# Kernel optimization log

Measured on AMD Instinct MI355X. Metric: run time of the kernel, lower is better.

Reference implementation:

```python
import jax, jax.numpy as jnp
import numpy as np

B, STATE_DIM, ACTION_DIM = 16384, 512, 64
HID, NQ, QED = 1024, 64, 64
EPS = 1e-5


def _layernorm(x, gamma, beta):
    mu = jnp.mean(x, axis=-1, keepdims=True)
    var = jnp.mean(jnp.square(x - mu), axis=-1, keepdims=True)
    return (x - mu) * jax.lax.rsqrt(var + EPS) * gamma + beta


def setup_inputs() -> dict:
    key = jax.random.key(0)
    ks = jax.random.split(key, 12)
    s = 0.02  # small init scale for stable activations
    return {
        "state": jax.random.normal(ks[0], (B, STATE_DIM), jnp.float32),
        "action": jax.random.normal(ks[1], (B, ACTION_DIM), jnp.float32),
        "W1": jax.random.normal(ks[2], (STATE_DIM + ACTION_DIM, HID), jnp.float32) * s,
        "b1": jax.random.normal(ks[3], (HID,), jnp.float32) * s,
        "g1": jnp.ones((HID,), jnp.float32),
        "be1": jnp.zeros((HID,), jnp.float32),
        "W2": jax.random.normal(ks[4], (HID, HID), jnp.float32) * s,
        "b2": jax.random.normal(ks[5], (HID,), jnp.float32) * s,
        "g2": jnp.ones((HID,), jnp.float32),
        "be2": jnp.zeros((HID,), jnp.float32),
        "Wq1": jax.random.normal(ks[6], (1, QED), jnp.float32) * s,
        "bq1": jax.random.normal(ks[7], (QED,), jnp.float32) * s,
        "Wq2": jax.random.normal(ks[8], (QED, QED), jnp.float32) * s,
        "bq2": jax.random.normal(ks[9], (QED,), jnp.float32) * s,
        "Wh": jax.random.normal(ks[10], (HID + QED, 1), jnp.float32) * s,
        "bh": jax.random.normal(ks[11], (1,), jnp.float32) * s,
    }


def reference(state, action, W1, b1, g1, be1, W2, b2, g2, be2,
              Wq1, bq1, Wq2, bq2, Wh, bh):
    # tau buffer: midpoints of NQ uniform bins
    tau = jnp.linspace(0.0, 1.0, NQ + 1)[:-1] + 1.0 / (2 * NQ)  # [NQ]

    # feature_net (Dropout is identity in eval)
    x = jnp.concatenate([state, action], axis=-1)               # [B, S+A]
    h = jax.nn.relu(_layernorm(x @ W1 + b1, g1, be1))           # [B, HID]
    h = jax.nn.relu(_layernorm(h @ W2 + b2, g2, be2))           # [B, HID]

    # quantile embedding: tau rows are batch-independent -> one [NQ, QED] MLP
    te = jax.nn.relu(tau[:, None] @ Wq1 + bq1) @ Wq2 + bq2      # [NQ, QED]

    # head on concat([features, tau_emb]) == split the head weight
    Wf, Wt = Wh[:HID, 0], Wh[HID:, 0]                           # [HID], [QED]
    quantiles = h @ Wf[:, None] + (te @ Wt)[None, :] + bh[0]    # [B, NQ]
    return quantiles
```

## Files before the change

### kernel.cpp

```cpp
#include <hip/hip_runtime.h>
#include <hip/hip_bf16.h>
#include <cstddef>

#define B_ROWS 16384
#define SDIM 512
#define ADIM 64
#define KDIM 576
#define HID 1024
#define NQ 64

#define T1_BLOCKS ((KDIM / 32) * (HID / 32))
#define T2_BLOCKS ((HID / 32) * (HID / 32))
#define PREP_BLOCKS (T1_BLOCKS + T2_BLOCKS + 1)

#define FK_LDS (16384 + 131072)

typedef __attribute__((ext_vector_type(8))) __bf16 bf16x8;
typedef __attribute__((ext_vector_type(4))) float f32x4;

static __device__ __forceinline__ float bf2f(unsigned short u) {
  union { unsigned int i; float f; } x; x.i = ((unsigned int)u) << 16; return x.f;
}
static __device__ __forceinline__ unsigned short f2bf(float f) {
  union { float f; unsigned int i; } x; x.f = f;
  unsigned int i = x.i + (0x7fffu + ((x.i >> 16) & 1u));
  return (unsigned short)(i >> 16);
}

static __device__ __forceinline__ void gload_lds16(const unsigned short* g, unsigned short* l) {
  __builtin_amdgcn_global_load_lds(
      (const __attribute__((address_space(1))) void*)(const void*)g,
      (__attribute__((address_space(3))) void*)(void*)l, 16, 0, 0);
}

static __device__ __forceinline__ uint4 pack8(float4 a, float4 b) {
  uint4 o;
  o.x = (unsigned)f2bf(a.x) | ((unsigned)f2bf(a.y) << 16);
  o.y = (unsigned)f2bf(a.z) | ((unsigned)f2bf(a.w) << 16);
  o.z = (unsigned)f2bf(b.x) | ((unsigned)f2bf(b.y) << 16);
  o.w = (unsigned)f2bf(b.z) | ((unsigned)f2bf(b.w) << 16);
  return o;
}

static __device__ __forceinline__ void transpose_body(
    const float* __restrict__ W, unsigned short* __restrict__ Wb,
    int Kin, int N, int k0, int n0, unsigned short* tile) {
  const int tx = threadIdx.x & 31, ty = threadIdx.x >> 5;
#pragma unroll
  for (int i = 0; i < 32; i += 8)
    tile[(ty + i) * 33 + tx] = f2bf(W[(size_t)(k0 + ty + i) * N + n0 + tx]);
  __syncthreads();
#pragma unroll
  for (int i = 0; i < 32; i += 8)
    Wb[(size_t)(n0 + ty + i) * Kin + k0 + tx] = tile[tx * 33 + ty + i];
}

__global__ __launch_bounds__(256) void prep_k(
    const float* __restrict__ W1, const float* __restrict__ W2,
    const float* __restrict__ Wq1, const float* __restrict__ bq1,
    const float* __restrict__ Wq2, const float* __restrict__ bq2,
    const float* __restrict__ Wh, const float* __restrict__ bh,
    unsigned short* __restrict__ w1b, unsigned short* __restrict__ w2b,
    float* __restrict__ qoff) {
  __shared__ unsigned short tile[32 * 33];
  const int b = blockIdx.x;
  if (b < T1_BLOCKS) {
    transpose_body(W1, w1b, KDIM, HID, (b / 32) * 32, (b % 32) * 32, tile);
  } else if (b < T1_BLOCKS + T2_BLOCKS) {
    const int t = b - T1_BLOCKS;
    transpose_body(W2, w2b, HID, HID, (t / 32) * 32, (t % 32) * 32, tile);
  } else {
    const int q = threadIdx.x;
    if (q < NQ) {
      const float tau = ((float)q + 0.5f) * (1.0f / (float)NQ);
      float t1[64];
#pragma unroll
      for (int k = 0; k < 64; ++k) t1[k] = fmaxf(fmaf(tau, Wq1[k], bq1[k]), 0.f);
      float acc = bh[0];
#pragma unroll 1
      for (int j = 0; j < 64; ++j) {
        float t2 = bq2[j];
#pragma unroll
        for (int k = 0; k < 64; ++k) t2 = fmaf(t1[k], Wq2[k * 64 + j], t2);
        acc = fmaf(t2, Wh[HID + j], acc);
      }
      qoff[q] = acc;
    }
  }
}

template <bool XSRC, bool FINAL>
__global__ __launch_bounds__(512, 2) void fused_k(
    const float* __restrict__ Xs,
    const float* __restrict__ Xa,
    const unsigned short* __restrict__ A,
    const unsigned short* __restrict__ Bt,
    const float* __restrict__ bias, const float* __restrict__ g,
    const float* __restrict__ be, const float* __restrict__ Wh,
    const float* __restrict__ qoff,
    unsigned short* __restrict__ Hout, float* __restrict__ Qout,
    int K, int NT) {
  extern __shared__ unsigned short sm[];
  __shared__ float part[8][64][2];
  __shared__ float murs[64][2];
  __shared__ float dotf[64];
  __shared__ float qof[64];

  const int tid = threadIdx.x;
  const int w = tid >> 6, l = tid & 63;
  const int r0 = (int)blockIdx.x * 64;
  const int sb = (int)blockIdx.x % NT;

  const int sce = ((((l & 7) << 4) ^ (((l >> 3) & 4) << 3)) >> 1);
  const int lr = (l & 15) << 7;
  const int cSw = (((l >> 4) << 4) ^ ((l & 4) << 3));

  f32x4 acc[4][8] = {};
  float4 ar0, ar1;

#define KT(x) ((((x) + sb) % NT) << 6)
#define AF(d, mi, kk) (*(const bf16x8*)(sm + (((d)*8192 + (mi)*2048 + lr + cSw + ((kk) << 6)) >> 1)))
#define BFW(ni, kk) (*(const bf16x8*)(sm + ((16384 + w*16384 + (ni)*2048 + lr + cSw + ((kk) << 6)) >> 1)))
#define ISSUE_A(d, kt) \
    gload_lds16(A + (size_t)(r0 + w * 8 + (l >> 3)) * K + (kt) + sce, \
                sm + (((d)*8192 + w * 1024) >> 1))
#define ALOADX(kt) do { \
    const int row_ = r0 + w * 8 + (l >> 3); \
    if ((kt) < SDIM) { const float* p_ = Xs + (size_t)row_ * SDIM + (kt) + sce; \
      ar0 = *(const float4*)p_; ar1 = *(const float4*)(p_ + 4); } \
    else { const float* p_ = Xa + (size_t)row_ * ADIM + ((kt) - SDIM) + sce; \
      ar0 = *(const float4*)p_; ar1 = *(const float4*)(p_ + 4); } } while (0)
#define AWRX(d) (*(uint4*)(sm + (((d)*8192 + w * 1024 + l * 16) >> 1)) = pack8(ar0, ar1))
#define ISSUE_B(kt) do { _Pragma("unroll") for (int i_ = 0; i_ < 16; ++i_) \
    gload_lds16(Bt + (size_t)(w * 128 + i_ * 8 + (l >> 3)) * K + (kt) + sce, \
                sm + ((16384 + w * 16384 + i_ * 1024) >> 1)); } while (0)
#define BAR() __builtin_amdgcn_s_barrier()
#define WAITLGKM() asm volatile("s_waitcnt lgkmcnt(0)" ::: "memory")
#define WAITVM(n) asm volatile("s_waitcnt vmcnt(" #n ")" ::: "memory")

  if (XSRC) {
    ALOADX(KT(0)); AWRX(0);
    ISSUE_B(KT(0));
    if (NT > 1) ALOADX(KT(1));
    WAITLGKM(); BAR();
  } else {
    ISSUE_A(0, KT(0));
    ISSUE_B(KT(0));
    ISSUE_A(1, KT(1));
    WAITVM(17); BAR();
  }

  for (int t = 0; t < NT; ++t) {
    const int d = t & 1;
    if (t + 1 < NT) { if (XSRC) { WAITVM(2); } else { WAITVM(1); } }
    else { WAITVM(0); }
    bf16x8 af[4], bfr[8];
#pragma unroll
    for (int mi = 0; mi < 4; ++mi) af[mi] = AF(d, mi, 0);
#pragma unroll
    for (int ni = 0; ni < 8; ++ni) bfr[ni] = BFW(ni, 0);
    __builtin_amdgcn_s_setprio(1);
#pragma unroll
    for (int mi = 0; mi < 4; ++mi)
#pragma unroll
      for (int ni = 0; ni < 8; ++ni)
        acc[mi][ni] = __builtin_amdgcn_mfma_f32_16x16x32_bf16(af[mi], bfr[ni], acc[mi][ni], 0, 0, 0);
    __builtin_amdgcn_s_setprio(0);
#pragma unroll
    for (int mi = 0; mi < 4; ++mi) af[mi] = AF(d, mi, 1);
#pragma unroll
    for (int ni = 0; ni < 8; ++ni) bfr[ni] = BFW(ni, 1);
    WAITLGKM();
    if (t + 1 < NT) ISSUE_B(KT(t + 1));
    if (XSRC && t + 1 < NT) AWRX((t + 1) & 1);
    __builtin_amdgcn_s_setprio(1);
#pragma unroll
    for (int mi = 0; mi < 4; ++mi)
#pragma unroll
      for (int ni = 0; ni < 8; ++ni)
        acc[mi][ni] = __builtin_amdgcn_mfma_f32_16x16x32_bf16(af[mi], bfr[ni], acc[mi][ni], 0, 0, 0);
    __builtin_amdgcn_s_setprio(0);
    if (XSRC) {
      if (t + 1 < NT) { WAITLGKM(); }
      BAR();
      if (t + 2 < NT) ALOADX(KT(t + 2));
    } else {
      if (t + 1 < NT) { WAITVM(16); }
      BAR();
      if (t + 2 < NT) ISSUE_A(d, KT(t + 2));
    }
  }

  float bcol[8], gcol[8], becol[8];
#pragma unroll
  for (int ni = 0; ni < 8; ++ni) {
    const int col = w * 128 + ni * 16 + (l & 15);
    bcol[ni] = bias[col];
    gcol[ni] = g[col];
    becol[ni] = be[col];
  }
#pragma unroll
  for (int mi = 0; mi < 4; ++mi)
#pragma unroll
    for (int rr = 0; rr < 4; ++rr) {
      float s1 = 0.f, s2 = 0.f;
#pragma unroll
      for (int ni = 0; ni < 8; ++ni) {
        const float x = acc[mi][ni][rr] + bcol[ni];
        s1 += x; s2 += x * x;
      }
#pragma unroll
      for (int o = 1; o < 16; o <<= 1) {
        s1 += __shfl_xor(s1, o, 64);
        s2 += __shfl_xor(s2, o, 64);
      }
      if ((l & 15) == 0) {
        const int row = mi * 16 + (l >> 4) * 4 + rr;
        part[w][row][0] = s1;
        part[w][row][1] = s2;
      }
    }
  __syncthreads();
  if (tid < 64) {
    float s1 = 0.f, s2 = 0.f;
#pragma unroll
    for (int ww = 0; ww < 8; ++ww) { s1 += part[ww][tid][0]; s2 += part[ww][tid][1]; }
    const float mu = s1 * (1.0f / HID);
    murs[tid][0] = mu;
    murs[tid][1] = rsqrtf(s2 * (1.0f / HID) - mu * mu + 1e-5f);
    if (FINAL) qof[tid] = qoff[tid];
  }
  __syncthreads();

  if (!FINAL) {
#pragma unroll
    for (int mi = 0; mi < 4; ++mi)
#pragma unroll
      for (int rr = 0; rr < 4; ++rr) {
        const int row = mi * 16 + (l >> 4) * 4 + rr;
        const float mu = murs[row][0], rs = murs[row][1];
        unsigned short* hp = Hout + (size_t)(r0 + row) * HID + w * 128 + (l & 15);
#pragma unroll
        for (int ni = 0; ni < 8; ++ni) {
          const float x = acc[mi][ni][rr] + bcol[ni];
          hp[ni * 16] = f2bf(fmaxf((x - mu) * rs * gcol[ni] + becol[ni], 0.f));
        }
      }
  } else {
    float wf[8];
#pragma unroll
    for (int ni = 0; ni < 8; ++ni) wf[ni] = Wh[w * 128 + ni * 16 + (l & 15)];
#pragma unroll
    for (int mi = 0; mi < 4; ++mi)
#pragma unroll
      for (int rr = 0; rr < 4; ++rr) {
        const int row = mi * 16 + (l >> 4) * 4 + rr;
        const float mu = murs[row][0], rs = murs[row][1];
        float dp = 0.f;
#pragma unroll
        for (int ni = 0; ni < 8; ++ni) {
          const float x = acc[mi][ni][rr] + bcol[ni];
          dp += fmaxf((x - mu) * rs * gcol[ni] + becol[ni], 0.f) * wf[ni];
        }
#pragma unroll
        for (int o = 1; o < 16; o <<= 1) dp += __shfl_xor(dp, o, 64);
        if ((l & 15) == 0) part[w][row][0] = dp;
      }
    __syncthreads();
    if (tid < 64) {
      float dsum = 0.f;
#pragma unroll
      for (int ww = 0; ww < 8; ++ww) dsum += part[ww][tid][0];
      dotf[tid] = dsum;
    }
    __syncthreads();
#pragma unroll
    for (int it = 0; it < 8; ++it) {
      const int idx = tid + it * 512;
      const int row = idx >> 6, q = idx & 63;
      Qout[(size_t)(r0 + row) * NQ + q] = dotf[row] + qof[q];
    }
  }
#undef KT
#undef AF
#undef BFW
#undef ISSUE_A
#undef ALOADX
#undef AWRX
#undef ISSUE_B
#undef BAR
#undef WAITLGKM
#undef WAITVM
}

extern "C" void kernel_launch(void* const* d_in, const int* in_sizes, int n_in,
                              void* d_out, int out_size, void* d_ws, size_t ws_size,
                              hipStream_t stream) {
  const float* state  = (const float*)d_in[0];
  const float* action = (const float*)d_in[1];
  const float* W1  = (const float*)d_in[2];
  const float* b1  = (const float*)d_in[3];
  const float* g1  = (const float*)d_in[4];
  const float* be1 = (const float*)d_in[5];
  const float* W2  = (const float*)d_in[6];
  const float* b2  = (const float*)d_in[7];
  const float* g2  = (const float*)d_in[8];
  const float* be2 = (const float*)d_in[9];
  const float* Wq1 = (const float*)d_in[10];
  const float* bq1 = (const float*)d_in[11];
  const float* Wq2 = (const float*)d_in[12];
  const float* bq2 = (const float*)d_in[13];
  const float* Wh  = (const float*)d_in[14];
  const float* bh  = (const float*)d_in[15];
  float* out = (float*)d_out;

  char* ws = (char*)d_ws;
  size_t off = 0;
  float* qoff = (float*)(ws + off); off += 256;
  unsigned short* w1b = (unsigned short*)(ws + off); off += (size_t)HID * KDIM * 2;
  unsigned short* w2b = (unsigned short*)(ws + off); off += (size_t)HID * HID * 2;
  unsigned short* h1b = (unsigned short*)(ws + off);

  (void)hipFuncSetAttribute((const void*)fused_k<true, false>, hipFuncAttributeMaxDynamicSharedMemorySize, FK_LDS);
  (void)hipFuncSetAttribute((const void*)fused_k<false, true>, hipFuncAttributeMaxDynamicSharedMemorySize, FK_LDS);

  prep_k<<<PREP_BLOCKS, 256, 0, stream>>>(W1, W2, Wq1, bq1, Wq2, bq2, Wh, bh,
                                          w1b, w2b, qoff);

  fused_k<true, false><<<B_ROWS / 64, 512, FK_LDS, stream>>>(
      state, action, nullptr, w1b, b1, g1, be1, nullptr, nullptr,
      h1b, nullptr, KDIM, KDIM / 64);
  fused_k<false, true><<<B_ROWS / 64, 512, FK_LDS, stream>>>(
      nullptr, nullptr, h1b, w2b, b2, g2, be2, Wh, qoff,
      nullptr, out, HID, HID / 64);
}
```

Before: 107.8 us.

## Load B fragments directly into registers and deepen A pipeline to eight stages

B-operand fragments are now read straight from global memory into registers, double-buffered by k-half, instead of being staged through LDS. This cuts LDS from about 144 KB to 64 KB. The freed LDS holds an 8-slot A ring with 4 tiles of lookahead and a barrier only every fourth K-step. NT becomes a template parameter so the loop can be fully unrolled. The cost is uncoalesced per-lane B loads from L2 and higher register pressure, since launch_bounds no longer asks for 2 blocks per SM.

```diff
diff --git a/kernel.cpp b/kernel.cpp
--- a/kernel.cpp
+++ b/kernel.cpp
@@ -13,7 +13,7 @@
 #define T2_BLOCKS ((HID / 32) * (HID / 32))
 #define PREP_BLOCKS (T1_BLOCKS + T2_BLOCKS + 1)
 
-#define FK_LDS (16384 + 131072)
+#define FK_LDS 65536
 
 typedef __attribute__((ext_vector_type(8))) __bf16 bf16x8;
 typedef __attribute__((ext_vector_type(4))) float f32x4;
@@ -89,8 +89,8 @@
   }
 }
 
-template <bool XSRC, bool FINAL>
-__global__ __launch_bounds__(512, 2) void fused_k(
+template <bool XSRC, bool FINAL, int NT>
+__global__ __launch_bounds__(512) void fused_k(
     const float* __restrict__ Xs,
     const float* __restrict__ Xa,
     const unsigned short* __restrict__ A,
@@ -99,7 +99,7 @@
     const float* __restrict__ be, const float* __restrict__ Wh,
     const float* __restrict__ qoff,
     unsigned short* __restrict__ Hout, float* __restrict__ Qout,
-    int K, int NT) {
+    int K) {
   extern __shared__ unsigned short sm[];
   __shared__ float part[8][64][2];
   __shared__ float murs[64][2];
@@ -116,81 +116,83 @@
   const int cSw = (((l >> 4) << 4) ^ ((l & 4) << 3));
 
   f32x4 acc[4][8] = {};
-  float4 ar0, ar1;
+  bf16x8 b0[8], b1[8];
+  float4 ar0, ar1, br0, br1;
+
+  const unsigned short* Bp = Bt + (size_t)(w * 128 + (l & 15)) * K + ((l >> 4) << 3);
 
 #define KT(x) ((((x) + sb) % NT) << 6)
 #define AF(d, mi, kk) (*(const bf16x8*)(sm + (((d)*8192 + (mi)*2048 + lr + cSw + ((kk) << 6)) >> 1)))
-#define BFW(ni, kk) (*(const bf16x8*)(sm + ((16384 + w*16384 + (ni)*2048 + lr + cSw + ((kk) << 6)) >> 1)))
 #define ISSUE_A(d, kt) \
     gload_lds16(A + (size_t)(r0 + w * 8 + (l >> 3)) * K + (kt) + sce, \
                 sm + (((d)*8192 + w * 1024) >> 1))
-#define ALOADX(kt) do { \
+#define ALOADX(q0, q1, kt) do { \
     const int row_ = r0 + w * 8 + (l >> 3); \
     if ((kt) < SDIM) { const float* p_ = Xs + (size_t)row_ * SDIM + (kt) + sce; \
-      ar0 = *(const float4*)p_; ar1 = *(const float4*)(p_ + 4); } \
+      q0 = *(const float4*)p_; q1 = *(const float4*)(p_ + 4); } \
     else { const float* p_ = Xa + (size_t)row_ * ADIM + ((kt) - SDIM) + sce; \
-      ar0 = *(const float4*)p_; ar1 = *(const float4*)(p_ + 4); } } while (0)
-#define AWRX(d) (*(uint4*)(sm + (((d)*8192 + w * 1024 + l * 16) >> 1)) = pack8(ar0, ar1))
-#define ISSUE_B(kt) do { _Pragma("unroll") for (int i_ = 0; i_ < 16; ++i_) \
-    gload_lds16(Bt + (size_t)(w * 128 + i_ * 8 + (l >> 3)) * K + (kt) + sce, \
-                sm + ((16384 + w * 16384 + i_ * 1024) >> 1)); } while (0)
+      q0 = *(const float4*)p_; q1 = *(const float4*)(p_ + 4); } } while (0)
+#define AWRX(d, q0, q1) (*(uint4*)(sm + (((d)*8192 + w * 1024 + l * 16) >> 1)) = pack8(q0, q1))
+#define LOADB(dst, kt, kk) do { _Pragma("unroll") for (int ni = 0; ni < 8; ++ni) \
+    dst[ni] = *(const bf16x8*)(Bp + (size_t)(ni * 16) * K + (kt) + (kk) * 32); } while (0)
 #define BAR() __builtin_amdgcn_s_barrier()
 #define WAITLGKM() asm volatile("s_waitcnt lgkmcnt(0)" ::: "memory")
-#define WAITVM(n) asm volatile("s_waitcnt vmcnt(" #n ")" ::: "memory")
+#define WAITVM16() asm volatile("s_waitcnt vmcnt(16)" ::: "memory")
 
   if (XSRC) {
-    ALOADX(KT(0)); AWRX(0);
-    ISSUE_B(KT(0));
-    if (NT > 1) ALOADX(KT(1));
+    ALOADX(ar0, ar1, KT(0)); ALOADX(br0, br1, KT(1));
+    AWRX(0, ar0, ar1);
+    ALOADX(ar0, ar1, KT(2));
+    AWRX(1, br0, br1);
+    ALOADX(br0, br1, KT(3));
+    AWRX(2, ar0, ar1);
+    AWRX(3, br0, br1);
+    LOADB(b0, KT(0), 0); LOADB(b1, KT(0), 1);
     WAITLGKM(); BAR();
   } else {
-    ISSUE_A(0, KT(0));
-    ISSUE_B(KT(0));
-    ISSUE_A(1, KT(1));
-    WAITVM(17); BAR();
-  }
-
+    ISSUE_A(0, KT(0)); ISSUE_A(1, KT(1)); ISSUE_A(2, KT(2)); ISSUE_A(3, KT(3));
+    LOADB(b0, KT(0), 0); LOADB(b1, KT(0), 1);
+    WAITVM16(); BAR();
+  }
+
+#pragma unroll
   for (int t = 0; t < NT; ++t) {
-    const int d = t & 1;
-    if (t + 1 < NT) { if (XSRC) { WAITVM(2); } else { WAITVM(1); } }
-    else { WAITVM(0); }
-    bf16x8 af[4], bfr[8];
+    const int d = t & 7;
+    bf16x8 af[4];
+    if (XSRC) {
+      if (t + 4 < NT) ALOADX(ar0, ar1, KT(t + 4));
+    } else {
+      if (t + 4 < NT) ISSUE_A((t + 4) & 7, KT(t + 4));
+    }
 #pragma unroll
     for (int mi = 0; mi < 4; ++mi) af[mi] = AF(d, mi, 0);
-#pragma unroll
-    for (int ni = 0; ni < 8; ++ni) bfr[ni] = BFW(ni, 0);
     __builtin_amdgcn_s_setprio(1);
 #pragma unroll
     for (int mi = 0; mi < 4; ++mi)
 #pragma unroll
       for (int ni = 0; ni < 8; ++ni)
-        acc[mi][ni] = __builtin_amdgcn_mfma_f32_16x16x32_bf16(af[mi], bfr[ni], acc[mi][ni], 0, 0, 0);
+        acc[mi][ni] = __builtin_amdgcn_mfma_f32_16x16x32_bf16(af[mi], b0[ni], acc[mi][ni], 0, 0, 0);
     __builtin_amdgcn_s_setprio(0);
+    if (t + 1 < NT) LOADB(b0, KT(t + 1), 0);
 #pragma unroll
     for (int mi = 0; mi < 4; ++mi) af[mi] = AF(d, mi, 1);
-#pragma unroll
-    for (int ni = 0; ni < 8; ++ni) bfr[ni] = BFW(ni, 1);
-    WAITLGKM();
-    if (t + 1 < NT) ISSUE_B(KT(t + 1));
-    if (XSRC && t + 1 < NT) AWRX((t + 1) & 1);
     __builtin_amdgcn_s_setprio(1);
 #pragma unroll
     for (int mi = 0; mi < 4; ++mi)
 #pragma unroll
       for (int ni = 0; ni < 8; ++ni)
-        acc[mi][ni] = __builtin_amdgcn_mfma_f32_16x16x32_bf16(af[mi], bfr[ni], acc[mi][ni], 0, 0, 0);
+        acc[mi][ni] = __builtin_amdgcn_mfma_f32_16x16x32_bf16(af[mi], b1[ni], acc[mi][ni], 0, 0, 0);
     __builtin_amdgcn_s_setprio(0);
-    if (XSRC) {
-      if (t + 1 < NT) { WAITLGKM(); }
+    if (t + 1 < NT) LOADB(b1, KT(t + 1), 1);
+    if (XSRC && t + 4 < NT) AWRX((t + 4) & 7, ar0, ar1);
+    if (((t & 3) == 3) && (t + 1 < NT)) {
+      if (XSRC) { WAITLGKM(); } 
+      WAITVM16();
       BAR();
-      if (t + 2 < NT) ALOADX(KT(t + 2));
-    } else {
-      if (t + 1 < NT) { WAITVM(16); }
-      BAR();
-      if (t + 2 < NT) ISSUE_A(d, KT(t + 2));
-    }
-  }
-
+    }
+  }
+
+  __syncthreads();
   float bcol[8], gcol[8], becol[8];
 #pragma unroll
   for (int ni = 0; ni < 8; ++ni) {
@@ -283,14 +285,13 @@
   }
 #undef KT
 #undef AF
-#undef BFW
 #undef ISSUE_A
 #undef ALOADX
 #undef AWRX
-#undef ISSUE_B
+#undef LOADB
 #undef BAR
 #undef WAITLGKM
-#undef WAITVM
+#undef WAITVM16
 }
 
 extern "C" void kernel_launch(void* const* d_in, const int* in_sizes, int n_in,
@@ -321,16 +322,18 @@
   unsigned short* w2b = (unsigned short*)(ws + off); off += (size_t)HID * HID * 2;
   unsigned short* h1b = (unsigned short*)(ws + off);
 
-  (void)hipFuncSetAttribute((const void*)fused_k<true, false>, hipFuncAttributeMaxDynamicSharedMemorySize, FK_LDS);
-  (void)hipFuncSetAttribute((const void*)fused_k<false, true>, hipFuncAttributeMaxDynamicSharedMemorySize, FK_LDS);
+  (void)hipFuncSetAttribute((const void*)fused_k<true, false, KDIM / 64>,
+                            hipFuncAttributeMaxDynamicSharedMemorySize, FK_LDS);
+  (void)hipFuncSetAttribute((const void*)fused_k<false, true, HID / 64>,
+                            hipFuncAttributeMaxDynamicSharedMemorySize, FK_LDS);
 
   prep_k<<<PREP_BLOCKS, 256, 0, stream>>>(W1, W2, Wq1, bq1, Wq2, bq2, Wh, bh,
                                           w1b, w2b, qoff);
 
-  fused_k<true, false><<<B_ROWS / 64, 512, FK_LDS, stream>>>(
+  fused_k<true, false, KDIM / 64><<<B_ROWS / 64, 512, FK_LDS, stream>>>(
       state, action, nullptr, w1b, b1, g1, be1, nullptr, nullptr,
-      h1b, nullptr, KDIM, KDIM / 64);
-  fused_k<false, true><<<B_ROWS / 64, 512, FK_LDS, stream>>>(
+      h1b, nullptr, KDIM);
+  fused_k<false, true, HID / 64><<<B_ROWS / 64, 512, FK_LDS, stream>>>(
       nullptr, nullptr, h1b, w2b, b2, g2, be2, Wh, qoff,
-      nullptr, out, HID, HID / 64);
-}
+      nullptr, out, HID);
+}
```

New measurement: 150.2 us. 1.39x slower.

## Fuse both MLP layers into one kernel, keeping hidden activations in LDS

Applied to the files above, without the earlier changes.

Merges the two GEMM+LayerNorm kernels into one. The first layer's normalized bf16 output for each 64-row tile stays in shared memory instead of going through global memory. The second GEMM streams W2 directly from global into registers, using a new permute kernel that lays W2 out in MFMA fragment order. This removes the h1 write and read round trip and one launch. The cost is an extra permute launch and second-layer B loads that are no longer staged in LDS, which may stall the MFMA pipeline on global latency.

```diff
diff --git a/kernel.cpp b/kernel.cpp
--- a/kernel.cpp
+++ b/kernel.cpp
@@ -8,6 +8,8 @@
 #define KDIM 576
 #define HID 1024
 #define NQ 64
+#define NT1 9
+#define NT2 16
 
 #define T1_BLOCKS ((KDIM / 32) * (HID / 32))
 #define T2_BLOCKS ((HID / 32) * (HID / 32))
@@ -89,17 +91,26 @@
   }
 }
 
-template <bool XSRC, bool FINAL>
-__global__ __launch_bounds__(512, 2) void fused_k(
-    const float* __restrict__ Xs,
-    const float* __restrict__ Xa,
-    const unsigned short* __restrict__ A,
-    const unsigned short* __restrict__ Bt,
-    const float* __restrict__ bias, const float* __restrict__ g,
-    const float* __restrict__ be, const float* __restrict__ Wh,
-    const float* __restrict__ qoff,
-    unsigned short* __restrict__ Hout, float* __restrict__ Qout,
-    int K, int NT) {
+__global__ __launch_bounds__(256) void w2perm_k(
+    const unsigned short* __restrict__ w2b, unsigned short* __restrict__ w2c) {
+  const int gt = blockIdx.x * 256 + threadIdx.x;
+  const int c = gt >> 6, l = gt & 63;
+  const int ni = c & 7, kk = (c >> 3) & 1, t = (c >> 4) & 15, w = c >> 8;
+  const int row = w * 128 + ni * 16 + (l & 15);
+  const int kcol = t * 64 + kk * 32 + ((l >> 4) << 3);
+  *(uint4*)(w2c + (size_t)gt * 8) = *(const uint4*)(w2b + (size_t)row * HID + kcol);
+}
+
+__global__ __launch_bounds__(512, 2) void fused_all_k(
+    const float* __restrict__ Xs, const float* __restrict__ Xa,
+    const unsigned short* __restrict__ B1t,
+    const unsigned short* __restrict__ w2c,
+    const float* __restrict__ b1, const float* __restrict__ g1,
+    const float* __restrict__ be1,
+    const float* __restrict__ b2, const float* __restrict__ g2,
+    const float* __restrict__ be2,
+    const float* __restrict__ Wh, const float* __restrict__ qoff,
+    float* __restrict__ Qout) {
   extern __shared__ unsigned short sm[];
   __shared__ float part[8][64][2];
   __shared__ float murs[64][2];
@@ -109,7 +120,7 @@
   const int tid = threadIdx.x;
   const int w = tid >> 6, l = tid & 63;
   const int r0 = (int)blockIdx.x * 64;
-  const int sb = (int)blockIdx.x % NT;
+  const int sb = (int)blockIdx.x % NT1;
 
   const int sce = ((((l & 7) << 4) ^ (((l >> 3) & 4) << 3)) >> 1);
   const int lr = (l & 15) << 7;
@@ -118,12 +129,9 @@
   f32x4 acc[4][8] = {};
   float4 ar0, ar1;
 
-#define KT(x) ((((x) + sb) % NT) << 6)
-#define AF(d, mi, kk) (*(const bf16x8*)(sm + (((d)*8192 + (mi)*2048 + lr + cSw + ((kk) << 6)) >> 1)))
-#define BFW(ni, kk) (*(const bf16x8*)(sm + ((16384 + w*16384 + (ni)*2048 + lr + cSw + ((kk) << 6)) >> 1)))
-#define ISSUE_A(d, kt) \
-    gload_lds16(A + (size_t)(r0 + w * 8 + (l >> 3)) * K + (kt) + sce, \
-                sm + (((d)*8192 + w * 1024) >> 1))
+#define KT(x) ((((x) + sb) % NT1) << 6)
+#define AF1(d, mi, kk) (*(const bf16x8*)(sm + (((d)*8192 + (mi)*2048 + lr + cSw + ((kk) << 6)) >> 1)))
+#define BF1(ni, kk) (*(const bf16x8*)(sm + ((16384 + w*16384 + ((l & 15) * 8 + (ni)) * 128 + (((l >> 4) << 4) ^ (((ni) & 4) << 3)) + ((kk) << 6)) >> 1)))
 #define ALOADX(kt) do { \
     const int row_ = r0 + w * 8 + (l >> 3); \
     if ((kt) < SDIM) { const float* p_ = Xs + (size_t)row_ * SDIM + (kt) + sce; \
@@ -131,74 +139,59 @@
     else { const float* p_ = Xa + (size_t)row_ * ADIM + ((kt) - SDIM) + sce; \
       ar0 = *(const float4*)p_; ar1 = *(const float4*)(p_ + 4); } } while (0)
 #define AWRX(d) (*(uint4*)(sm + (((d)*8192 + w * 1024 + l * 16) >> 1)) = pack8(ar0, ar1))
-#define ISSUE_B(kt) do { _Pragma("unroll") for (int i_ = 0; i_ < 16; ++i_) \
-    gload_lds16(Bt + (size_t)(w * 128 + i_ * 8 + (l >> 3)) * K + (kt) + sce, \
+#define ISSUE_B1(kt) do { _Pragma("unroll") for (int i_ = 0; i_ < 16; ++i_) \
+    gload_lds16(B1t + (size_t)(w * 128 + i_ * 8 + (l >> 3)) * KDIM + (kt) + sce, \
                 sm + ((16384 + w * 16384 + i_ * 1024) >> 1)); } while (0)
+#define AF2(t, mi, kk) (*(const bf16x8*)(sm + ((16384 + ((t) >> 1) * 16384 + ((t) & 1) * 8192 + (mi)*2048 + lr + cSw + ((kk) << 6)) >> 1)))
+#define LOADB2H(dst, t, kk, h) do { _Pragma("unroll") for (int j_ = 0; j_ < 4; ++j_) \
+    dst[j_] = *(const bf16x8*)(w2c + ((size_t)((((w * NT2 + (t)) * 2 + (kk)) * 8 + (h) * 4 + j_) * 64 + l) * 8)); } while (0)
+#define MQ1(bsrc) do { _Pragma("unroll") for (int mi = 0; mi < 4; ++mi) \
+    _Pragma("unroll") for (int ni = 0; ni < 8; ++ni) \
+      acc[mi][ni] = __builtin_amdgcn_mfma_f32_16x16x32_bf16(af[mi], bsrc[ni], acc[mi][ni], 0, 0, 0); } while (0)
+#define MQ2(cv, NO) do { _Pragma("unroll") for (int mi = 0; mi < 4; ++mi) \
+    _Pragma("unroll") for (int j_ = 0; j_ < 4; ++j_) \
+      acc[mi][(NO) + j_] = __builtin_amdgcn_mfma_f32_16x16x32_bf16(af2[mi], cv[j_], acc[mi][(NO) + j_], 0, 0, 0); } while (0)
 #define BAR() __builtin_amdgcn_s_barrier()
 #define WAITLGKM() asm volatile("s_waitcnt lgkmcnt(0)" ::: "memory")
 #define WAITVM(n) asm volatile("s_waitcnt vmcnt(" #n ")" ::: "memory")
-
-  if (XSRC) {
-    ALOADX(KT(0)); AWRX(0);
-    ISSUE_B(KT(0));
-    if (NT > 1) ALOADX(KT(1));
-    WAITLGKM(); BAR();
-  } else {
-    ISSUE_A(0, KT(0));
-    ISSUE_B(KT(0));
-    ISSUE_A(1, KT(1));
-    WAITVM(17); BAR();
-  }
-
-  for (int t = 0; t < NT; ++t) {
+#define PRIO1() __builtin_amdgcn_s_setprio(1)
+#define PRIO0() __builtin_amdgcn_s_setprio(0)
+
+  ALOADX(KT(0)); AWRX(0);
+  ISSUE_B1(KT(0));
+  ALOADX(KT(1));
+  WAITLGKM(); BAR();
+
+  for (int t = 0; t < NT1; ++t) {
     const int d = t & 1;
-    if (t + 1 < NT) { if (XSRC) { WAITVM(2); } else { WAITVM(1); } }
-    else { WAITVM(0); }
+    if (t + 1 < NT1) { WAITVM(2); } else { WAITVM(0); }
     bf16x8 af[4], bfr[8];
 #pragma unroll
-    for (int mi = 0; mi < 4; ++mi) af[mi] = AF(d, mi, 0);
-#pragma unroll
-    for (int ni = 0; ni < 8; ++ni) bfr[ni] = BFW(ni, 0);
-    __builtin_amdgcn_s_setprio(1);
-#pragma unroll
-    for (int mi = 0; mi < 4; ++mi)
-#pragma unroll
-      for (int ni = 0; ni < 8; ++ni)
-        acc[mi][ni] = __builtin_amdgcn_mfma_f32_16x16x32_bf16(af[mi], bfr[ni], acc[mi][ni], 0, 0, 0);
-    __builtin_amdgcn_s_setprio(0);
-#pragma unroll
-    for (int mi = 0; mi < 4; ++mi) af[mi] = AF(d, mi, 1);
-#pragma unroll
-    for (int ni = 0; ni < 8; ++ni) bfr[ni] = BFW(ni, 1);
+    for (int mi = 0; mi < 4; ++mi) af[mi] = AF1(d, mi, 0);
+#pragma unroll
+    for (int ni = 0; ni < 8; ++ni) bfr[ni] = BF1(ni, 0);
+    PRIO1(); MQ1(bfr); PRIO0();
+#pragma unroll
+    for (int mi = 0; mi < 4; ++mi) af[mi] = AF1(d, mi, 1);
+#pragma unroll
+    for (int ni = 0; ni < 8; ++ni) bfr[ni] = BF1(ni, 1);
     WAITLGKM();
-    if (t + 1 < NT) ISSUE_B(KT(t + 1));
-    if (XSRC && t + 1 < NT) AWRX((t + 1) & 1);
-    __builtin_amdgcn_s_setprio(1);
-#pragma unroll
-    for (int mi = 0; mi < 4; ++mi)
-#pragma unroll
-      for (int ni = 0; ni < 8; ++ni)
-        acc[mi][ni] = __builtin_amdgcn_mfma_f32_16x16x32_bf16(af[mi], bfr[ni], acc[mi][ni], 0, 0, 0);
-    __builtin_amdgcn_s_setprio(0);
-    if (XSRC) {
-      if (t + 1 < NT) { WAITLGKM(); }
-      BAR();
-      if (t + 2 < NT) ALOADX(KT(t + 2));
-    } else {
-      if (t + 1 < NT) { WAITVM(16); }
-      BAR();
-      if (t + 2 < NT) ISSUE_A(d, KT(t + 2));
-    }
+    if (t + 1 < NT1) ISSUE_B1(KT(t + 1));
+    if (t + 1 < NT1) AWRX((t + 1) & 1);
+    PRIO1(); MQ1(bfr); PRIO0();
+    if (t + 1 < NT1) { WAITLGKM(); }
+    BAR();
+    if (t + 2 < NT1) ALOADX(KT(t + 2));
   }
 
   float bcol[8], gcol[8], becol[8];
-#pragma unroll
-  for (int ni = 0; ni < 8; ++ni) {
-    const int col = w * 128 + ni * 16 + (l & 15);
-    bcol[ni] = bias[col];
-    gcol[ni] = g[col];
-    becol[ni] = be[col];
-  }
+  const int cb = w * 128 + (l & 15) * 8;
+  *(float4*)&bcol[0]  = *(const float4*)(b1 + cb);
+  *(float4*)&bcol[4]  = *(const float4*)(b1 + cb + 4);
+  *(float4*)&gcol[0]  = *(const float4*)(g1 + cb);
+  *(float4*)&gcol[4]  = *(const float4*)(g1 + cb + 4);
+  *(float4*)&becol[0] = *(const float4*)(be1 + cb);
+  *(float4*)&becol[4] = *(const float4*)(be1 + cb + 4);
 #pragma unroll
   for (int mi = 0; mi < 4; ++mi)
 #pragma unroll
@@ -228,66 +221,132 @@
     const float mu = s1 * (1.0f / HID);
     murs[tid][0] = mu;
     murs[tid][1] = rsqrtf(s2 * (1.0f / HID) - mu * mu + 1e-5f);
-    if (FINAL) qof[tid] = qoff[tid];
-  }
-  __syncthreads();
-
-  if (!FINAL) {
-#pragma unroll
-    for (int mi = 0; mi < 4; ++mi)
-#pragma unroll
-      for (int rr = 0; rr < 4; ++rr) {
+    qof[tid] = qoff[tid];
+  }
+  __syncthreads();
+#pragma unroll
+  for (int mi = 0; mi < 4; ++mi)
+#pragma unroll
+    for (int rr = 0; rr < 4; ++rr) {
+      const int row = mi * 16 + (l >> 4) * 4 + rr;
+      const float mu = murs[row][0], rs = murs[row][1];
+      uint4 ov;
+      unsigned int* op = (unsigned int*)&ov;
+#pragma unroll
+      for (int i = 0; i < 4; ++i) {
+        const float y0 = fmaxf((acc[mi][2 * i][rr] + bcol[2 * i] - mu) * rs * gcol[2 * i] + becol[2 * i], 0.f);
+        const float y1 = fmaxf((acc[mi][2 * i + 1][rr] + bcol[2 * i + 1] - mu) * rs * gcol[2 * i + 1] + becol[2 * i + 1], 0.f);
+        op[i] = (unsigned)f2bf(y0) | ((unsigned)f2bf(y1) << 16);
+      }
+      *(uint4*)(sm + ((16384 + w * 16384 + ((l & 15) >> 3) * 8192 + row * 128
+                       + (((l & 7) * 16) ^ ((row & 4) << 3))) >> 1)) = ov;
+    }
+  __syncthreads();
+
+#pragma unroll
+  for (int mi = 0; mi < 4; ++mi)
+#pragma unroll
+    for (int ni = 0; ni < 8; ++ni) acc[mi][ni] = (f32x4){0.f, 0.f, 0.f, 0.f};
+
+  {
+    bf16x8 ca[4], cbf[4], af2[4];
+    LOADB2H(ca, 0, 0, 0);
+    for (int t = 0; t < NT2; ++t) {
+#pragma unroll
+      for (int mi = 0; mi < 4; ++mi) af2[mi] = AF2(t, mi, 0);
+      LOADB2H(cbf, t, 0, 1);
+      PRIO1(); MQ2(ca, 0); PRIO0();
+      LOADB2H(ca, t, 1, 0);
+      PRIO1(); MQ2(cbf, 4); PRIO0();
+#pragma unroll
+      for (int mi = 0; mi < 4; ++mi) af2[mi] = AF2(t, mi, 1);
+      LOADB2H(cbf, t, 1, 1);
+      PRIO1(); MQ2(ca, 0); PRIO0();
+      if (t + 1 < NT2) LOADB2H(ca, t + 1, 0, 0);
+      PRIO1(); MQ2(cbf, 4); PRIO0();
+    }
+  }
+
+  float b2c[8], g2c[8], be2c[8], wf[8];
+#pragma unroll
+  for (int ni = 0; ni < 8; ++ni) {
+    const int col = w * 128 + ni * 16 + (l & 15);
+    b2c[ni] = b2[col];
+    g2c[ni] = g2[col];
+    be2c[ni] = be2[col];
+    wf[ni] = Wh[col];
+  }
+#pragma unroll
+  for (int mi = 0; mi < 4; ++mi)
+#pragma unroll
+    for (int rr = 0; rr < 4; ++rr) {
+      float s1 = 0.f, s2 = 0.f;
+#pragma unroll
+      for (int ni = 0; ni < 8; ++ni) {
+        const float x = acc[mi][ni][rr] + b2c[ni];
+        s1 += x; s2 += x * x;
+      }
+#pragma unroll
+      for (int o = 1; o < 16; o <<= 1) {
+        s1 += __shfl_xor(s1, o, 64);
+        s2 += __shfl_xor(s2, o, 64);
+      }
+      if ((l & 15) == 0) {
         const int row = mi * 16 + (l >> 4) * 4 + rr;
-        const float mu = murs[row][0], rs = murs[row][1];
-        unsigned short* hp = Hout + (size_t)(r0 + row) * HID + w * 128 + (l & 15);
-#pragma unroll
-        for (int ni = 0; ni < 8; ++ni) {
-          const float x = acc[mi][ni][rr] + bcol[ni];
-          hp[ni * 16] = f2bf(fmaxf((x - mu) * rs * gcol[ni] + becol[ni], 0.f));
-        }
-      }
-  } else {
-    float wf[8];
-#pragma unroll
-    for (int ni = 0; ni < 8; ++ni) wf[ni] = Wh[w * 128 + ni * 16 + (l & 15)];
-#pragma unroll
-    for (int mi = 0; mi < 4; ++mi)
-#pragma unroll
-      for (int rr = 0; rr < 4; ++rr) {
-        const int row = mi * 16 + (l >> 4) * 4 + rr;
-        const float mu = murs[row][0], rs = murs[row][1];
-        float dp = 0.f;
-#pragma unroll
-        for (int ni = 0; ni < 8; ++ni) {
-          const float x = acc[mi][ni][rr] + bcol[ni];
-          dp += fmaxf((x - mu) * rs * gcol[ni] + becol[ni], 0.f) * wf[ni];
-        }
-#pragma unroll
-        for (int o = 1; o < 16; o <<= 1) dp += __shfl_xor(dp, o, 64);
-        if ((l & 15) == 0) part[w][row][0] = dp;
-      }
-    __syncthreads();
-    if (tid < 64) {
-      float dsum = 0.f;
-#pragma unroll
-      for (int ww = 0; ww < 8; ++ww) dsum += part[ww][tid][0];
-      dotf[tid] = dsum;
-    }
-    __syncthreads();
-#pragma unroll
-    for (int it = 0; it < 8; ++it) {
-      const int idx = tid + it * 512;
-      const int row = idx >> 6, q = idx & 63;
-      Qout[(size_t)(r0 + row) * NQ + q] = dotf[row] + qof[q];
-    }
+        part[w][row][0] = s1;
+        part[w][row][1] = s2;
+      }
+    }
+  __syncthreads();
+  if (tid < 64) {
+    float s1 = 0.f, s2 = 0.f;
+#pragma unroll
+    for (int ww = 0; ww < 8; ++ww) { s1 += part[ww][tid][0]; s2 += part[ww][tid][1]; }
+    const float mu = s1 * (1.0f / HID);
+    murs[tid][0] = mu;
+    murs[tid][1] = rsqrtf(s2 * (1.0f / HID) - mu * mu + 1e-5f);
+  }
+  __syncthreads();
+#pragma unroll
+  for (int mi = 0; mi < 4; ++mi)
+#pragma unroll
+    for (int rr = 0; rr < 4; ++rr) {
+      const int row = mi * 16 + (l >> 4) * 4 + rr;
+      const float mu = murs[row][0], rs = murs[row][1];
+      float dp = 0.f;
+#pragma unroll
+      for (int ni = 0; ni < 8; ++ni) {
+        const float x = acc[mi][ni][rr] + b2c[ni];
+        dp += fmaxf((x - mu) * rs * g2c[ni] + be2c[ni], 0.f) * wf[ni];
+      }
+#pragma unroll
+      for (int o = 1; o < 16; o <<= 1) dp += __shfl_xor(dp, o, 64);
+      if ((l & 15) == 0) part[w][row][0] = dp;
+    }
+  __syncthreads();
+  if (tid < 64) {
+    float dsum = 0.f;
+#pragma unroll
+    for (int ww = 0; ww < 8; ++ww) dsum += part[ww][tid][0];
+    dotf[tid] = dsum;
+  }
+  __syncthreads();
+#pragma unroll
+  for (int it = 0; it < 8; ++it) {
+    const int idx = tid + it * 512;
+    const int row = idx >> 6, q = idx & 63;
+    Qout[(size_t)(r0 + row) * NQ + q] = dotf[row] + qof[q];
   }
 #undef KT
-#undef AF
-#undef BFW
-#undef ISSUE_A
+#undef AF1
+#undef BF1
 #undef ALOADX
 #undef AWRX
-#undef ISSUE_B
+#undef ISSUE_B1
+#undef AF2
+#undef LOADB2H
+#undef MQ1
+#undef MQ2
 #undef BAR
 #undef WAITLGKM
 #undef WAITVM
@@ -319,18 +378,15 @@
   float* qoff = (float*)(ws + off); off += 256;
   unsigned short* w1b = (unsigned short*)(ws + off); off += (size_t)HID * KDIM * 2;
   unsigned short* w2b = (unsigned short*)(ws + off); off += (size_t)HID * HID * 2;
-  unsigned short* h1b = (unsigned short*)(ws + off);
-
-  (void)hipFuncSetAttribute((const void*)fused_k<true, false>, hipFuncAttributeMaxDynamicSharedMemorySize, FK_LDS);
-  (void)hipFuncSetAttribute((const void*)fused_k<false, true>, hipFuncAttributeMaxDynamicSharedMemorySize, FK_LDS);
+  unsigned short* w2c = (unsigned short*)(ws + off);
+
+  (void)hipFuncSetAttribute((const void*)fused_all_k,
+                            hipFuncAttributeMaxDynamicSharedMemorySize, FK_LDS);
 
   prep_k<<<PREP_BLOCKS, 256, 0, stream>>>(W1, W2, Wq1, bq1, Wq2, bq2, Wh, bh,
                                           w1b, w2b, qoff);
-
-  fused_k<true, false><<<B_ROWS / 64, 512, FK_LDS, stream>>>(
-      state, action, nullptr, w1b, b1, g1, be1, nullptr, nullptr,
-      h1b, nullptr, KDIM, KDIM / 64);
-  fused_k<false, true><<<B_ROWS / 64, 512, FK_LDS, stream>>>(
-      nullptr, nullptr, h1b, w2b, b2, g2, be2, Wh, qoff,
-      nullptr, out, HID, HID / 64);
-}
+  w2perm_k<<<512, 256, 0, stream>>>(w2b, w2c);
+
+  fused_all_k<<<B_ROWS / 64, 512, FK_LDS, stream>>>(
+      state, action, w1b, w2c, b1, g1, be1, b2, g2, be2, Wh, qoff, out);
+}
```

Result: no change. 107.4 us (-0.3%).
